# Optimization experiments

Hardware: AMD Instinct MI355X
Metric: run time of the kernel (lower is better)

Reference implementation:

```python
import jax, jax.numpy as jnp
import numpy as np

BN_EPS = 1e-3  # Keras BatchNormalization default epsilon


def _conv_block(x, k):
    """Per-task conv (stride 2, pad 1) -> ReLU -> BatchNorm (center/scale=False, training).

    x: [B, E, H, W, Cin]  (B tasks, E examples per task)
    k: [B, kh, kw, Cin, Cout]  per-task kernel
    """
    def conv_one(xe, kt):  # xe: [E,H,W,Cin], kt: [kh,kw,Cin,Cout]
        return jax.lax.conv_general_dilated(
            xe, kt, window_strides=(2, 2), padding=[(1, 1), (1, 1)],
            dimension_numbers=('NHWC', 'HWIO', 'NHWC'))
    y = jax.nn.relu(jax.vmap(conv_one)(x, k))  # [B,E,H',W',Cout]
    # BatchNorm in training mode: moments over all axes except channels
    m = jnp.mean(y, axis=(0, 1, 2, 3))
    v = jnp.var(y, axis=(0, 1, 2, 3))
    return (y - m) * jax.lax.rsqrt(v + BN_EPS)


def setup_inputs() -> dict:
    key = jax.random.key(0)
    ks = jax.random.split(key, 6)
    B, E, H, C, O = 64, 64, 28, 64, 20
    return {
        'x': jax.random.normal(ks[0], (B, E, H, H, 1), dtype=jnp.float32),
        'k1': jax.random.normal(ks[1], (B, 3, 3, 1, C), dtype=jnp.float32) * 0.1,
        'k2': jax.random.normal(ks[2], (B, 3, 3, C, C), dtype=jnp.float32) * 0.05,
        'k3': jax.random.normal(ks[3], (B, 3, 3, C, C), dtype=jnp.float32) * 0.05,
        'k4': jax.random.normal(ks[4], (B, 3, 3, C, C), dtype=jnp.float32) * 0.05,
        'w_ro': jax.random.normal(ks[5], (B, C, O), dtype=jnp.float32) * 0.1,
    }


def reference(x, k1, k2, k3, k4, w_ro):
    h = _conv_block(x, k1)   # [B,E,14,14,C]
    h = _conv_block(h, k2)   # [B,E,7,7,C]
    h = _conv_block(h, k3)   # [B,E,4,4,C]
    h = _conv_block(h, k4)   # [B,E,2,2,C]
    # MaxPooling2D with pool size == full spatial extent -> global spatial max
    feat = jnp.max(h, axis=(2, 3))  # [B,E,C]
    # per-task readout matmul: [B,E,H] x [B,H,O] -> [B,E,O]
    return jnp.einsum('beh,bho->beo', feat, w_ro)
```

## Files before the change

kernel.cpp:

```cpp
#include <hip/hip_runtime.h>

#define BN_EPS 1e-3f

typedef __attribute__((ext_vector_type(8))) short bf16x8;
typedef __attribute__((ext_vector_type(16))) float floatx16;
typedef unsigned short u16;

__device__ __forceinline__ u16 f2bf(float f) {
  unsigned u = __float_as_uint(f);
  u += 0x7fffu + ((u >> 16) & 1u);
  return (u16)(u >> 16);
}
__device__ __forceinline__ float bf2f(u16 h) {
  return __uint_as_float(((unsigned)h) << 16);
}

static constexpr int NSHARD = 64;

__global__ __launch_bounds__(256) void conv1_k(
    const float* __restrict__ x, const float* __restrict__ k1,
    u16* __restrict__ y1, float* __restrict__ statsSh)
{
  __shared__ float xp[30 * 32];
  __shared__ float w1s[576];
  __shared__ float redsum[64], redss[64];

  const int be = blockIdx.x, b = be >> 6, tid = threadIdx.x;

  for (int i = tid; i < 960; i += 256) xp[i] = 0.f;
  for (int i = tid; i < 576; i += 256) w1s[i] = k1[(size_t)b * 576 + i];
  if (tid < 64) { redsum[tid] = 0.f; redss[tid] = 0.f; }
  __syncthreads();
  for (int i = tid; i < 784; i += 256) {
    const int r = i / 28, c = i - 28 * r;
    xp[(r + 1) * 32 + (c + 1)] = x[(size_t)be * 784 + i];
  }
  __syncthreads();

  if (tid < 224) {
    const int oy = tid >> 4, cg = (tid & 15) * 4;
    float w[4][9];
#pragma unroll
    for (int cc = 0; cc < 4; ++cc)
#pragma unroll
      for (int t = 0; t < 9; ++t) w[cc][t] = w1s[t * 64 + cg + cc];

    float xr[3][29];
#pragma unroll
    for (int ky = 0; ky < 3; ++ky)
#pragma unroll
      for (int j = 0; j < 29; ++j) xr[ky][j] = xp[(2 * oy + ky) * 32 + j];

    float sum[4] = {0.f, 0.f, 0.f, 0.f}, ss[4] = {0.f, 0.f, 0.f, 0.f};
#pragma unroll
    for (int ox = 0; ox < 14; ++ox) {
      alignas(8) u16 o[4];
#pragma unroll
      for (int cc = 0; cc < 4; ++cc) {
        float a = 0.f;
#pragma unroll
        for (int ky = 0; ky < 3; ++ky)
#pragma unroll
          for (int kx = 0; kx < 3; ++kx)
            a = fmaf(xr[ky][2 * ox + kx], w[cc][ky * 3 + kx], a);
        const float v = fmaxf(a, 0.f);
        o[cc] = f2bf(v);
        sum[cc] += v;
        ss[cc] = fmaf(v, v, ss[cc]);
      }
      *(uint2*)&y1[((size_t)be * 196 + oy * 14 + ox) * 64 + cg] = *(uint2*)o;
    }
#pragma unroll
    for (int cc = 0; cc < 4; ++cc) {
      atomicAdd(&redsum[cg + cc], sum[cc]);
      atomicAdd(&redss[cg + cc], ss[cc]);
    }
  }
  __syncthreads();
  if (tid < 64) {
    const int sh = be & (NSHARD - 1);
    atomicAdd(&statsSh[sh * 128 + tid], redsum[tid]);
    atomicAdd(&statsSh[sh * 128 + 64 + tid], redss[tid]);
  }
}

__global__ __launch_bounds__(256) void foldw_k(
    const float* __restrict__ W, const float* __restrict__ statsSh, float invN,
    u16* __restrict__ Wf, float* __restrict__ biasCls)
{
  __shared__ float T[64 * 68];
  __shared__ float P[256];
  __shared__ float s1[64], t1[64];
  __shared__ float tbS[64];

  const int b = blockIdx.x / 3, sg = blockIdx.x % 3;
  const int tid = threadIdx.x;

  {
    const int g = tid >> 7, cidx = tid & 127;
    float acc = 0.f;
    for (int k = 0; k < NSHARD / 2; ++k)
      acc += statsSh[(g * (NSHARD / 2) + k) * 128 + cidx];
    P[tid] = acc;
  }
  __syncthreads();
  if (tid < 64) {
    const float m = (P[tid] + P[tid + 128]) * invN;
    const float var = fmaf(-m, m, (P[64 + tid] + P[192 + tid]) * invN);
    const float s = rsqrtf(var + BN_EPS);
    s1[tid] = s;
    t1[tid] = -m * s;
  }
  __syncthreads();

  const int cin = tid >> 2, q0 = (tid & 3) * 16;
  const int cout = tid >> 2, ci0 = (tid & 3) * 16;
  for (int s = sg * 3; s < sg * 3 + 3; ++s) {
    if (tid < 64) tbS[tid] = 0.f;
    const float* ss = W + ((size_t)b * 9 + s) * 4096;
#pragma unroll
    for (int q = 0; q < 16; q += 4) {
      const float4 v = *(const float4*)(ss + cin * 64 + q0 + q);
      T[(q0 + q + 0) * 68 + cin] = v.x;
      T[(q0 + q + 1) * 68 + cin] = v.y;
      T[(q0 + q + 2) * 68 + cin] = v.z;
      T[(q0 + q + 3) * 68 + cin] = v.w;
    }
    __syncthreads();
    alignas(16) u16 tmp[16];
    float tb = 0.f;
#pragma unroll
    for (int j = 0; j < 16; ++j) {
      const float wv = T[cout * 68 + ci0 + j];
      tmp[j] = f2bf(wv * s1[ci0 + j]);
      tb = fmaf(t1[ci0 + j], wv, tb);
    }
    u16* dst = Wf + ((size_t)b * 9 + s) * 4096 + cout * 64 + ci0;
    *(uint4*)dst       = *(uint4*)&tmp[0];
    *(uint4*)(dst + 8) = *(uint4*)&tmp[8];
    atomicAdd(&tbS[cout], tb);
    __syncthreads();
    if (tid < 64) {
      const int ky = s / 3, kx = s % 3;
      const float tv = tbS[tid];
#pragma unroll
      for (int cls = 0; cls < 9; ++cls) {
        const int ry = cls / 3, rx = cls % 3;
        const bool valid = !((ry == 1 && ky == 0) || (ry == 2 && ky == 2) ||
                             (rx == 1 && kx == 0) || (rx == 2 && kx == 2));
        if (valid) atomicAdd(&biasCls[(size_t)b * 576 + cls * 64 + tid], tv);
      }
    }
    __syncthreads();
  }
}

template <int Hin, int Hout, int G>
__device__ __forceinline__ void conv_core(
    const u16* __restrict__ yin, const u16* __restrict__ Wf,
    const float* __restrict__ biasCls, u16* __restrict__ yout,
    float* __restrict__ statsSh, int blk)
{
  constexpr int PPI  = Hout * Hout;
  constexpr int ROWS = G * PPI;
  constexpr int BPT  = 64 / G;
  constexpr int MR   = G * Hin * Hin;
  constexpr int ZR   = MR;

  __shared__ __align__(16) u16 mapS[(MR + 1) * 72];
  __shared__ __align__(16) u16 Bb[2][64 * 72];
  __shared__ float biasS[576];
  __shared__ float redsum[64], redss[64];

  const int b = blk / BPT, e0 = (blk % BPT) * G;
  const int tid = threadIdx.x, lane = tid & 63, wave = tid >> 6;

  for (int i = tid; i < 576; i += 256) biasS[i] = biasCls[(size_t)b * 576 + i];
  if (tid < 64) { redsum[tid] = 0.f; redss[tid] = 0.f; }
  if (tid < 8) *(uint4*)&mapS[ZR * 72 + tid * 8] = uint4{0, 0, 0, 0};

  {
    const u16* src = yin + (size_t)(b * 64 + e0) * (Hin * Hin) * 64;
    for (int ch = tid; ch < MR * 8; ch += 256) {
      const int r = ch >> 3, c8 = ch & 7;
      *(uint4*)&mapS[r * 72 + c8 * 8] = *(const uint4*)(src + ch * 8);
    }
  }

  const int bco = tid >> 2, bci = (tid & 3) * 16;
  const u16* wb = Wf + (size_t)b * 9 * 4096 + bco * 64 + bci;
  {
    uint4 b0 = *(const uint4*)wb;
    uint4 b1 = *(const uint4*)(wb + 8);
    *(uint4*)&Bb[0][bco * 72 + bci]     = b0;
    *(uint4*)&Bb[0][bco * 72 + bci + 8] = b1;
  }

  const int m0 = (wave & 1) * 32, n0 = (wave >> 1) * 32;
  const int l31 = lane & 31, kq = (lane >> 5) * 8;
  const int lrow = m0 + l31;
  const bool rv = lrow < ROWS;
  const int img = rv ? lrow / PPI : 0;
  const int pp  = rv ? lrow % PPI : 0;
  const int oy = pp / Hout, ox = pp % Hout;

  floatx16 acc;
#pragma unroll
  for (int r = 0; r < 16; ++r) acc[r] = 0.f;

  __syncthreads();

#pragma unroll
  for (int s = 0; s < 9; ++s) {
    uint4 nb0, nb1;
    if (s < 8) {
      const u16* wsl = wb + (s + 1) * 4096;
      nb0 = *(const uint4*)wsl;
      nb1 = *(const uint4*)(wsl + 8);
    }
    const int ky = s / 3, kx = s % 3;
    int pix = ZR;
    if (rv) {
      const int iy = 2 * oy - 1 + ky, ix = 2 * ox - 1 + kx;
      if ((unsigned)iy < (unsigned)Hin && (unsigned)ix < (unsigned)Hin)
        pix = img * (Hin * Hin) + iy * Hin + ix;
    }
    const u16* ap = &mapS[pix * 72 + kq];
    const u16* bp = &Bb[s & 1][(n0 + l31) * 72 + kq];
#pragma unroll
    for (int kk = 0; kk < 4; ++kk) {
      bf16x8 a  = *(const bf16x8*)(ap + kk * 16);
      bf16x8 bv = *(const bf16x8*)(bp + kk * 16);
      acc = __builtin_amdgcn_mfma_f32_32x32x16_bf16(a, bv, acc, 0, 0, 0);
    }
    if (s < 8) {
      u16* d = &Bb[(s + 1) & 1][bco * 72 + bci];
      *(uint4*)d       = nb0;
      *(uint4*)(d + 8) = nb1;
    }
    __syncthreads();
  }

  const int col = n0 + l31;
  const int rb = m0 + 4 * (lane >> 5);
  float ls = 0.f, lss = 0.f;
#pragma unroll
  for (int r = 0; r < 16; ++r) {
    const int rw = rb + (r & 3) + 8 * (r >> 2);
    if (rw < ROWS) {
      const int re = rw / PPI, pr = rw % PPI;
      const int ooy = pr / Hout, oox = pr % Hout;
      const int ry = (ooy == 0) ? 1 : ((2 * ooy + 1 >= Hin) ? 2 : 0);
      const int rx = (oox == 0) ? 1 : ((2 * oox + 1 >= Hin) ? 2 : 0);
      const float v = fmaxf(acc[r] + biasS[(ry * 3 + rx) * 64 + col], 0.f);
      yout[((size_t)(b * 64 + e0 + re) * PPI + pr) * 64 + col] = f2bf(v);
      ls += v;
      lss = fmaf(v, v, lss);
    }
  }
  atomicAdd(&redsum[col], ls);
  atomicAdd(&redss[col], lss);
  __syncthreads();
  if (tid < 64) {
    const int sh = blk & (NSHARD - 1);
    atomicAdd(&statsSh[sh * 128 + tid], redsum[tid]);
    atomicAdd(&statsSh[sh * 128 + 64 + tid], redss[tid]);
  }
}

__global__ __launch_bounds__(256) void cg2_k(
    const u16* __restrict__ yin, const u16* __restrict__ Wf,
    const float* __restrict__ biasCls, u16* __restrict__ yout,
    float* __restrict__ statsSh) {
  conv_core<14, 7, 1>(yin, Wf, biasCls, yout, statsSh, blockIdx.x);
}
__global__ __launch_bounds__(256) void cg3_k(
    const u16* __restrict__ yin, const u16* __restrict__ Wf,
    const float* __restrict__ biasCls, u16* __restrict__ yout,
    float* __restrict__ statsSh) {
  conv_core<7, 4, 4>(yin, Wf, biasCls, yout, statsSh, blockIdx.x);
}
__global__ __launch_bounds__(256) void cg4_k(
    const u16* __restrict__ yin, const u16* __restrict__ Wf,
    const float* __restrict__ biasCls, u16* __restrict__ yout,
    float* __restrict__ statsSh) {
  conv_core<4, 2, 16>(yin, Wf, biasCls, yout, statsSh, blockIdx.x);
}

__global__ __launch_bounds__(256) void readout_k(
    const u16* __restrict__ y4, const float* __restrict__ w_ro,
    const float* __restrict__ statsSh, float invN, float* __restrict__ outp)
{
  __shared__ float wl[64 * 20];
  __shared__ float feat[64 * 64];
  __shared__ float P[256];
  __shared__ float sArr[64], tArr[64];

  const int b = blockIdx.x, tid = threadIdx.x;

  {
    const int g = tid >> 7, cidx = tid & 127;
    float acc = 0.f;
    for (int k = 0; k < NSHARD / 2; ++k)
      acc += statsSh[(g * (NSHARD / 2) + k) * 128 + cidx];
    P[tid] = acc;
  }
  for (int i = tid; i < 1280; i += 256) wl[i] = w_ro[(size_t)b * 1280 + i];
  __syncthreads();
  if (tid < 64) {
    const float m = (P[tid] + P[tid + 128]) * invN;
    const float var = fmaf(-m, m, (P[64 + tid] + P[192 + tid]) * invN);
    const float s = rsqrtf(var + BN_EPS);
    sArr[tid] = s;
    tArr[tid] = -m * s;
  }
  __syncthreads();

  {
    const int e = tid & 63;
    for (int c = tid >> 6; c < 64; c += 4) {
      const u16* p4 = y4 + ((size_t)(b * 64 + e) * 4) * 64 + c;
      const float v = fmaxf(fmaxf(bf2f(p4[0]), bf2f(p4[64])),
                            fmaxf(bf2f(p4[128]), bf2f(p4[192])));
      feat[c * 64 + e] = fmaf(v, sArr[c], tArr[c]);
    }
  }
  __syncthreads();

  const int e = tid >> 2, og = (tid & 3) * 5;
  float acc[5] = {0.f, 0.f, 0.f, 0.f, 0.f};
  for (int c = 0; c < 64; ++c) {
    const float f = feat[c * 64 + e];
#pragma unroll
    for (int j = 0; j < 5; ++j) acc[j] = fmaf(f, wl[c * 20 + og + j], acc[j]);
  }
#pragma unroll
  for (int j = 0; j < 5; ++j)
    outp[((size_t)b * 64 + e) * 20 + og + j] = acc[j];
}

extern "C" void kernel_launch(void* const* d_in, const int* in_sizes, int n_in,
                              void* d_out, int out_size, void* d_ws, size_t ws_size,
                              hipStream_t stream) {
  (void)in_sizes; (void)n_in; (void)out_size; (void)ws_size;
  const float* x   = (const float*)d_in[0];
  const float* k1  = (const float*)d_in[1];
  const float* k2  = (const float*)d_in[2];
  const float* k3  = (const float*)d_in[3];
  const float* k4  = (const float*)d_in[4];
  const float* wro = (const float*)d_in[5];
  float* out = (float*)d_out;
  char* ws = (char*)d_ws;

  float* stats = (float*)ws;
  float* bias2 = (float*)(ws + 131072);
  float* bias3 = bias2 + 36864;
  float* bias4 = bias3 + 36864;
  u16* k2f = (u16*)(ws + 131072 + 442368);
  u16* k3f = k2f + (size_t)2359296;
  u16* k4f = k3f + (size_t)2359296;
  u16* y2 = k4f + (size_t)2359296;
  u16* y1 = y2 + (size_t)12845056;
  u16* y3 = y1;
  u16* y4 = y3 + (size_t)4194304;

  float* st1 = stats;
  float* st2 = stats + 8192;
  float* st3 = stats + 16384;
  float* st4 = stats + 24576;

  hipMemsetAsync(stats, 0, 131072 + 442368, stream);

  conv1_k<<<4096, 256, 0, stream>>>(x, k1, y1, st1);
  foldw_k<<<192, 256, 0, stream>>>(k2, st1, 1.f / 802816.f, k2f, bias2);
  cg2_k<<<4096, 256, 0, stream>>>(y1, k2f, bias2, y2, st2);
  foldw_k<<<192, 256, 0, stream>>>(k3, st2, 1.f / 200704.f, k3f, bias3);
  cg3_k<<<1024, 256, 0, stream>>>(y2, k3f, bias3, y3, st3);
  foldw_k<<<192, 256, 0, stream>>>(k4, st3, 1.f / 65536.f, k4f, bias4);
  cg4_k<<<256, 256, 0, stream>>>(y3, k4f, bias4, y4, st4);
  readout_k<<<64, 256, 0, stream>>>(y4, wro, st4, 1.f / 16384.f, out);
}
```

Baseline: 263.7 us.

## Compute first conv layer with split-bf16 MFMA instead of scalar FMAs

Rewrites the first 3x3 conv (Cin=1) as an im2col GEMM per image: patches and weights are split into hi/lo bf16 parts in shared memory and multiplied with three 32x32x16 bf16 MFMAs per tile to approximate fp32 accuracy. This replaces the per-thread scalar FMA loop over register-cached rows. In exchange it adds LDS staging, conversion work and scattered 2-byte output stores instead of packed 8-byte stores. It also sets a launch-bounds occupancy hint.

```diff
diff --git a/kernel.cpp b/kernel.cpp
--- a/kernel.cpp
+++ b/kernel.cpp
@@ -17,64 +17,112 @@
 
 static constexpr int NSHARD = 64;
 
-__global__ __launch_bounds__(256) void conv1_k(
+__global__ __launch_bounds__(256, 4) void conv1_k(
     const float* __restrict__ x, const float* __restrict__ k1,
     u16* __restrict__ y1, float* __restrict__ statsSh)
 {
-  __shared__ float xp[30 * 32];
-  __shared__ float w1s[576];
+  __shared__ __align__(16) u16 Ah[256 * 24];
+  __shared__ __align__(16) u16 Al[256 * 24];
+  __shared__ __align__(16) u16 Wh[64 * 24];
+  __shared__ __align__(16) u16 Wl[64 * 24];
+  __shared__ __align__(16) float xp[30 * 36];
   __shared__ float redsum[64], redss[64];
 
   const int be = blockIdx.x, b = be >> 6, tid = threadIdx.x;
 
-  for (int i = tid; i < 960; i += 256) xp[i] = 0.f;
-  for (int i = tid; i < 576; i += 256) w1s[i] = k1[(size_t)b * 576 + i];
-  if (tid < 64) { redsum[tid] = 0.f; redss[tid] = 0.f; }
-  __syncthreads();
+  {
+    const uint4 z = uint4{0, 0, 0, 0};
+    for (int i = tid; i < 768; i += 256) ((uint4*)Ah)[i] = z;
+    for (int i = tid; i < 768; i += 256) ((uint4*)Al)[i] = z;
+    if (tid < 192) ((uint4*)Wh)[tid] = z;
+    if (tid < 192) ((uint4*)Wl)[tid] = z;
+    for (int i = tid; i < 270; i += 256) ((uint4*)xp)[i] = z;
+    if (tid < 64) { redsum[tid] = 0.f; redss[tid] = 0.f; }
+  }
+  __syncthreads();
+
   for (int i = tid; i < 784; i += 256) {
     const int r = i / 28, c = i - 28 * r;
-    xp[(r + 1) * 32 + (c + 1)] = x[(size_t)be * 784 + i];
-  }
-  __syncthreads();
-
-  if (tid < 224) {
-    const int oy = tid >> 4, cg = (tid & 15) * 4;
-    float w[4][9];
-#pragma unroll
-    for (int cc = 0; cc < 4; ++cc)
-#pragma unroll
-      for (int t = 0; t < 9; ++t) w[cc][t] = w1s[t * 64 + cg + cc];
-
-    float xr[3][29];
+    xp[(r + 1) * 36 + (c + 1)] = x[(size_t)be * 784 + i];
+  }
+  for (int idx = tid; idx < 576; idx += 256) {
+    const int t = idx >> 6, c = idx & 63;
+    const float v = k1[(size_t)b * 576 + idx];
+    const u16 hi = f2bf(v);
+    const u16 lo = f2bf(v - bf2f(hi));
+    Wh[c * 24 + t] = hi;
+    Wl[c * 24 + t] = lo;
+  }
+  __syncthreads();
+
+  if (tid < 196) {
+    const int oy = tid / 14, ox = tid - 14 * oy;
+    const float* base = &xp[(2 * oy) * 36 + 2 * ox];
 #pragma unroll
     for (int ky = 0; ky < 3; ++ky)
 #pragma unroll
-      for (int j = 0; j < 29; ++j) xr[ky][j] = xp[(2 * oy + ky) * 32 + j];
-
-    float sum[4] = {0.f, 0.f, 0.f, 0.f}, ss[4] = {0.f, 0.f, 0.f, 0.f};
-#pragma unroll
-    for (int ox = 0; ox < 14; ++ox) {
-      alignas(8) u16 o[4];
-#pragma unroll
-      for (int cc = 0; cc < 4; ++cc) {
-        float a = 0.f;
-#pragma unroll
-        for (int ky = 0; ky < 3; ++ky)
-#pragma unroll
-          for (int kx = 0; kx < 3; ++kx)
-            a = fmaf(xr[ky][2 * ox + kx], w[cc][ky * 3 + kx], a);
-        const float v = fmaxf(a, 0.f);
-        o[cc] = f2bf(v);
-        sum[cc] += v;
-        ss[cc] = fmaf(v, v, ss[cc]);
+      for (int kx = 0; kx < 3; ++kx) {
+        const float v = base[ky * 36 + kx];
+        const u16 hi = f2bf(v);
+        const u16 lo = f2bf(v - bf2f(hi));
+        Ah[tid * 24 + ky * 3 + kx] = hi;
+        Al[tid * 24 + ky * 3 + kx] = lo;
       }
-      *(uint2*)&y1[((size_t)be * 196 + oy * 14 + ox) * 64 + cg] = *(uint2*)o;
-    }
-#pragma unroll
-    for (int cc = 0; cc < 4; ++cc) {
-      atomicAdd(&redsum[cg + cc], sum[cc]);
-      atomicAdd(&redss[cg + cc], ss[cc]);
-    }
+  }
+  __syncthreads();
+
+  const int wave = tid >> 6, lane = tid & 63;
+  const int l31 = lane & 31, kq = (lane >> 5) * 8;
+
+  bf16x8 ah[2], al[2], bh[2], bl[2];
+#pragma unroll
+  for (int mt = 0; mt < 2; ++mt) {
+    const int row = (wave * 2 + mt) * 32 + l31;
+    ah[mt] = *(const bf16x8*)&Ah[row * 24 + kq];
+    al[mt] = *(const bf16x8*)&Al[row * 24 + kq];
+  }
+#pragma unroll
+  for (int nt = 0; nt < 2; ++nt) {
+    const int colB = nt * 32 + l31;
+    bh[nt] = *(const bf16x8*)&Wh[colB * 24 + kq];
+    bl[nt] = *(const bf16x8*)&Wl[colB * 24 + kq];
+  }
+
+  floatx16 acc[2][2];
+#pragma unroll
+  for (int mt = 0; mt < 2; ++mt)
+#pragma unroll
+    for (int nt = 0; nt < 2; ++nt) {
+#pragma unroll
+      for (int r = 0; r < 16; ++r) acc[mt][nt][r] = 0.f;
+      acc[mt][nt] = __builtin_amdgcn_mfma_f32_32x32x16_bf16(
+          al[mt], bh[nt], acc[mt][nt], 0, 0, 0);
+      acc[mt][nt] = __builtin_amdgcn_mfma_f32_32x32x16_bf16(
+          ah[mt], bl[nt], acc[mt][nt], 0, 0, 0);
+      acc[mt][nt] = __builtin_amdgcn_mfma_f32_32x32x16_bf16(
+          ah[mt], bh[nt], acc[mt][nt], 0, 0, 0);
+    }
+
+#pragma unroll
+  for (int nt = 0; nt < 2; ++nt) {
+    const int col = nt * 32 + l31;
+    float ls = 0.f, lss = 0.f;
+#pragma unroll
+    for (int mt = 0; mt < 2; ++mt) {
+      const int rb = (wave * 2 + mt) * 32 + 4 * (lane >> 5);
+#pragma unroll
+      for (int r = 0; r < 16; ++r) {
+        const int rw = rb + (r & 3) + 8 * (r >> 2);
+        if (rw < 196) {
+          const float v = fmaxf(acc[mt][nt][r], 0.f);
+          y1[((size_t)be * 196 + rw) * 64 + col] = f2bf(v);
+          ls += v;
+          lss = fmaf(v, v, lss);
+        }
+      }
+    }
+    atomicAdd(&redsum[col], ls);
+    atomicAdd(&redss[col], lss);
   }
   __syncthreads();
   if (tid < 64) {
```

Measured after the change: 254.3 us. 3.6% less time.
